# Optimization experiments

Hardware: AMD Instinct MI355X
Metric: run time of the kernel (lower is better)

## Reference

```python
import jax, jax.numpy as jnp
import numpy as np

L, B, I, H = 1024, 128, 256, 512

def setup_inputs() -> dict:
    key = jax.random.key(0)
    k1, k2, k3, k4, k5 = jax.random.split(key, 5)
    s_i = 1.0 / np.sqrt(I)
    s_h = 1.0 / np.sqrt(H)
    return {
        "x": jax.random.normal(k1, (L, B, I), dtype=jnp.float32),
        "h": jax.random.normal(k2, (B, H), dtype=jnp.float32),
        "Wx": jax.random.uniform(k3, (H, I), jnp.float32, -s_i, s_i),
        "Wh": jax.random.uniform(k4, (H, H), jnp.float32, -s_h, s_h),
        "bh": jax.random.uniform(k5, (H,), jnp.float32, -s_h, s_h),
    }

def reference(x, h, Wx, Wh, bh):
    # Precompute input projection for all timesteps as one big GEMM:
    # (L,B,I) @ (I,H) -> (L,B,H)
    xproj = jnp.einsum("lbi,hi->lbh", x, Wx)

    def step(h_prev, xp_t):
        h_new = jnp.tanh(xp_t + h_prev @ Wh.T + bh)  # (B,H)
        return h_new, h_new

    _, h_seq = jax.lax.scan(step, h, xproj)
    return h_seq  # (L, B, H)
```

## Files before the change

kernel.cpp:

```cpp
#include <hip/hip_runtime.h>

#define L_DIM 1024
#define B_DIM 128
#define I_DIM 256
#define H_DIM 512

typedef unsigned short u16x8 __attribute__((ext_vector_type(8)));
typedef __bf16 bf16x8 __attribute__((ext_vector_type(8)));
typedef float f32x4 __attribute__((ext_vector_type(4)));
typedef unsigned long long u64;
typedef unsigned int u32;
typedef u64 u64x2 __attribute__((ext_vector_type(2)));

static __device__ __forceinline__ unsigned short f2bf(float f) {
  unsigned u = __builtin_bit_cast(unsigned, f);
  u += 0x7FFFu + ((u >> 16) & 1u);
  return (unsigned short)(u >> 16);
}
static __device__ __forceinline__ float bf2f(unsigned short b) {
  return __builtin_bit_cast(float, ((unsigned)b) << 16);
}
static __device__ __forceinline__ bf16x8 ld_frag_g(const unsigned short* p, size_t idx8) {
  return __builtin_bit_cast(bf16x8, reinterpret_cast<const u16x8*>(p)[idx8]);
}

__global__ void pack_weights(const float* __restrict__ Wx, const float* __restrict__ Wh,
                             unsigned short* __restrict__ WxHi, unsigned short* __restrict__ WxLo,
                             unsigned short* __restrict__ WhHi, unsigned short* __restrict__ WhLo) {
  int tid = blockIdx.x * blockDim.x + threadIdx.x;
  if (tid < 32 * 8 * 64) {
    int lane = tid & 63, kt = (tid >> 6) & 7, nt = tid >> 9;
    int n = nt * 16 + (lane & 15), k0 = kt * 32 + (lane >> 4) * 8;
    const float* src = Wx + (size_t)n * I_DIM + k0;
    #pragma unroll
    for (int j = 0; j < 8; ++j) {
      float v = src[j];
      unsigned short hb = f2bf(v);
      WxHi[(size_t)tid * 8 + j] = hb;
      WxLo[(size_t)tid * 8 + j] = f2bf(v - bf2f(hb));
    }
  }
  if (tid < 32 * 16 * 64) {
    int lane = tid & 63, kt = (tid >> 6) & 15, nt = tid >> 10;
    int n = nt * 16 + (lane & 15), k0 = kt * 32 + (lane >> 4) * 8;
    const float* src = Wh + (size_t)n * H_DIM + k0;
    #pragma unroll
    for (int j = 0; j < 8; ++j) {
      float v = src[j];
      unsigned short hb = f2bf(v);
      WhHi[(size_t)tid * 8 + j] = hb;
      WhLo[(size_t)tid * 8 + j] = f2bf(v - bf2f(hb));
    }
  }
}

__global__ __launch_bounds__(256) void xproj_kernel(const float* __restrict__ x,
    const unsigned short* __restrict__ WxHi, const unsigned short* __restrict__ WxLo,
    const float* __restrict__ bh, float* __restrict__ out) {
  __shared__ unsigned short ahi[128][40];
  __shared__ unsigned short alo[128][40];
  const int tid = threadIdx.x, lane = tid & 63, wid = tid >> 6;
  const int mbase = blockIdx.x * 128, cbase = blockIdx.y * 128;
  const int wrow = (wid >> 1) * 64, wcol = (wid & 1) * 64;
  f32x4 acc[4][4] = {};
  const int srow = tid >> 1, shalf = (tid & 1) * 16;

  for (int kt = 0; kt < 8; ++kt) {
    const f32x4* src = reinterpret_cast<const f32x4*>(
        x + (size_t)(mbase + srow) * I_DIM + kt * 32 + shalf);
    f32x4 v[4];
    v[0] = src[0]; v[1] = src[1]; v[2] = src[2]; v[3] = src[3];
    u16x8 hh[2], ll[2];
    #pragma unroll
    for (int q = 0; q < 2; ++q) {
      #pragma unroll
      for (int e = 0; e < 8; ++e) {
        float f = v[q * 2 + (e >> 2)][e & 3];
        unsigned short hb = f2bf(f);
        hh[q][e] = hb;
        ll[q][e] = f2bf(f - bf2f(hb));
      }
    }
    __syncthreads();
    *reinterpret_cast<u16x8*>(&ahi[srow][shalf]) = hh[0];
    *reinterpret_cast<u16x8*>(&ahi[srow][shalf + 8]) = hh[1];
    *reinterpret_cast<u16x8*>(&alo[srow][shalf]) = ll[0];
    *reinterpret_cast<u16x8*>(&alo[srow][shalf + 8]) = ll[1];
    __syncthreads();

    bf16x8 amh[4], aml[4];
    #pragma unroll
    for (int m = 0; m < 4; ++m) {
      amh[m] = __builtin_bit_cast(bf16x8, *reinterpret_cast<const u16x8*>(
          &ahi[wrow + m * 16 + (lane & 15)][(lane >> 4) * 8]));
      aml[m] = __builtin_bit_cast(bf16x8, *reinterpret_cast<const u16x8*>(
          &alo[wrow + m * 16 + (lane & 15)][(lane >> 4) * 8]));
    }
    bf16x8 bhh[4], bll[4];
    #pragma unroll
    for (int n = 0; n < 4; ++n) {
      int ntg = (cbase + wcol) / 16 + n;
      size_t idx = (size_t)(ntg * 8 + kt) * 64 + lane;
      bhh[n] = ld_frag_g(WxHi, idx);
      bll[n] = ld_frag_g(WxLo, idx);
    }
    #pragma unroll
    for (int m = 0; m < 4; ++m) {
      #pragma unroll
      for (int n = 0; n < 4; ++n) {
        acc[m][n] = __builtin_amdgcn_mfma_f32_16x16x32_bf16(amh[m], bhh[n], acc[m][n], 0, 0, 0);
        acc[m][n] = __builtin_amdgcn_mfma_f32_16x16x32_bf16(aml[m], bhh[n], acc[m][n], 0, 0, 0);
        acc[m][n] = __builtin_amdgcn_mfma_f32_16x16x32_bf16(amh[m], bll[n], acc[m][n], 0, 0, 0);
      }
    }
  }

  #pragma unroll
  for (int n = 0; n < 4; ++n) {
    int col = cbase + wcol + n * 16 + (lane & 15);
    float bv = bh[col];
    #pragma unroll
    for (int m = 0; m < 4; ++m) {
      int rg = mbase + wrow + m * 16 + ((lane >> 4) << 2);
      #pragma unroll
      for (int r = 0; r < 4; ++r)
        out[(size_t)(rg + r) * H_DIM + col] = acc[m][n][r] + bv;
    }
  }
}

__global__ __launch_bounds__(64, 1) void rnn_kernel(const float* __restrict__ h0,
    const unsigned short* __restrict__ WhHi, const unsigned short* __restrict__ WhLo,
    u32* __restrict__ tags, unsigned short* __restrict__ slab,
    float* __restrict__ out) {
  const int lane = threadIdx.x & 63;
  const int b = blockIdx.x;
  const int g = b & 7, c = (b >> 3) & 7, w = (b >> 6) & 3;
  const int cw = c * 4 + w;

  bf16x8 wfh[16], wfl[16];
  #pragma unroll
  for (int kt = 0; kt < 16; ++kt) {
    size_t idx = (size_t)(cw * 16 + kt) * 64 + lane;
    wfh[kt] = ld_frag_g(WhHi, idx);
    wfl[kt] = ld_frag_g(WhLo, idx);
  }

  const int arow = lane & 15;
  const int aoff = (lane >> 4) * 8;
  const int drow = (lane >> 4) * 4;
  const int gcol = c * 64 + w * 16 + (lane & 15);
  const int koff2 = (lane >> 4) * 2;

  bf16x8 af[16];
  #pragma unroll
  for (int kt = 0; kt < 16; ++kt) {
    const f32x4* hp = reinterpret_cast<const f32x4*>(
        h0 + (size_t)(g * 16 + arow) * H_DIM + kt * 32 + aoff);
    f32x4 v0 = hp[0], v1 = hp[1];
    u16x8 hv;
    #pragma unroll
    for (int e = 0; e < 4; ++e) { hv[e] = f2bf(v0[e]); hv[4 + e] = f2bf(v1[e]); }
    af[kt] = __builtin_bit_cast(bf16x8, hv);
  }

  f32x4 xpv;
  #pragma unroll
  for (int r = 0; r < 4; ++r)
    xpv[r] = out[(size_t)(g * 16 + drow + r) * H_DIM + gcol];

  for (int t = 0; t < L_DIM; ++t) {
    const size_t obase = ((size_t)t * B_DIM + g * 16) * H_DIM;

    f32x4 a0 = {}, a1 = {}, a2 = {}, a3 = {};
    #pragma unroll
    for (int kt = 0; kt < 16; kt += 2) {
      a0 = __builtin_amdgcn_mfma_f32_16x16x32_bf16(af[kt], wfh[kt], a0, 0, 0, 0);
      a1 = __builtin_amdgcn_mfma_f32_16x16x32_bf16(af[kt], wfl[kt], a1, 0, 0, 0);
      a2 = __builtin_amdgcn_mfma_f32_16x16x32_bf16(af[kt + 1], wfh[kt + 1], a2, 0, 0, 0);
      a3 = __builtin_amdgcn_mfma_f32_16x16x32_bf16(af[kt + 1], wfl[kt + 1], a3, 0, 0, 0);
    }

    float hv[4]; unsigned short hu[4];
    #pragma unroll
    for (int r = 0; r < 4; ++r) {
      float z = a0[r] + a1[r] + a2[r] + a3[r] + xpv[r];
      float e = __expf(2.0f * z);
      hv[r] = 1.0f - 2.0f / (e + 1.0f);
      hu[r] = f2bf(hv[r]);
    }

    if (t < L_DIM - 1) {
      const unsigned step = (unsigned)(t + 1);
      const unsigned buf = step & 1;
      unsigned short* sg = slab + (size_t)(buf * 8 + g) * 8192;

      #pragma unroll
      for (int r = 0; r < 4; ++r)
        __hip_atomic_store(&sg[(drow + r) * H_DIM + gcol], hu[r],
                           __ATOMIC_RELAXED, __HIP_MEMORY_SCOPE_AGENT);
      __builtin_amdgcn_sched_barrier(0);
      asm volatile("s_waitcnt vmcnt(0)" ::: "memory");
      __builtin_amdgcn_sched_barrier(0);
      if (lane == 0)
        __hip_atomic_store(tags + ((size_t)(buf * 8 + g) * 32 + cw) * 16, step,
                           __ATOMIC_RELAXED, __HIP_MEMORY_SCOPE_AGENT);

      #pragma unroll
      for (int r = 0; r < 4; ++r)
        out[obase + (size_t)(drow + r) * H_DIM + gcol] = hv[r];
      const size_t obn = ((size_t)(t + 1) * B_DIM + g * 16) * H_DIM;
      #pragma unroll
      for (int r = 0; r < 4; ++r)
        xpv[r] = out[obn + (size_t)(drow + r) * H_DIM + gcol];

      if (lane < 32) {
        const u32* tp = tags + ((size_t)(buf * 8 + g) * 32 + lane) * 16;
        while (__hip_atomic_load(tp, __ATOMIC_RELAXED, __HIP_MEMORY_SCOPE_AGENT) < step) {}
      }
      __builtin_amdgcn_sched_barrier(0);
      asm volatile("" ::: "memory");

      const u64* sp = reinterpret_cast<const u64*>(sg);
      #pragma unroll
      for (int kt = 0; kt < 16; ++kt) {
        const u64* p = sp + arow * 128 + kt * 8 + koff2;
        u64x2 pv;
        pv[0] = __hip_atomic_load(p, __ATOMIC_RELAXED, __HIP_MEMORY_SCOPE_AGENT);
        pv[1] = __hip_atomic_load(p + 1, __ATOMIC_RELAXED, __HIP_MEMORY_SCOPE_AGENT);
        af[kt] = __builtin_bit_cast(bf16x8, pv);
      }
    } else {
      #pragma unroll
      for (int r = 0; r < 4; ++r)
        out[obase + (size_t)(drow + r) * H_DIM + gcol] = hv[r];
    }
  }
}

extern "C" void kernel_launch(void* const* d_in, const int* in_sizes, int n_in,
                              void* d_out, int out_size, void* d_ws, size_t ws_size,
                              hipStream_t stream) {
  (void)in_sizes; (void)n_in; (void)out_size; (void)ws_size;
  const float* x  = (const float*)d_in[0];
  const float* h0 = (const float*)d_in[1];
  const float* Wx = (const float*)d_in[2];
  const float* Wh = (const float*)d_in[3];
  const float* bh = (const float*)d_in[4];
  float* out = (float*)d_out;

  unsigned short* WxHi = (unsigned short*)d_ws;
  unsigned short* WxLo = WxHi + 131072;
  unsigned short* WhHi = WxLo + 131072;
  unsigned short* WhLo = WhHi + 262144;
  unsigned short* slab = (unsigned short*)((char*)d_ws + 1572864);
  u32*            tags = (u32*)((char*)d_ws + 1835008);

  hipMemsetAsync(tags, 0, 32768, stream);

  hipLaunchKernelGGL(pack_weights, dim3(128), dim3(256), 0, stream,
                     Wx, Wh, WxHi, WxLo, WhHi, WhLo);
  hipLaunchKernelGGL(xproj_kernel, dim3(1024, 4), dim3(256), 0, stream,
                     x, WxHi, WxLo, bh, out);
  hipLaunchKernelGGL(rnn_kernel, dim3(256), dim3(64), 0, stream,
                     h0, WhHi, WhLo, tags, slab, out);
}
```

Measured before the change: 3.220 ms.

## Embed step tags in slab data words to replace separate flag synchronization

```diff
diff --git a/kernel.cpp b/kernel.cpp
--- a/kernel.cpp
+++ b/kernel.cpp
@@ -10,7 +10,6 @@
 typedef float f32x4 __attribute__((ext_vector_type(4)));
 typedef unsigned long long u64;
 typedef unsigned int u32;
-typedef u64 u64x2 __attribute__((ext_vector_type(2)));
 
 static __device__ __forceinline__ unsigned short f2bf(float f) {
   unsigned u = __builtin_bit_cast(unsigned, f);
@@ -131,12 +130,10 @@
 
 __global__ __launch_bounds__(64, 1) void rnn_kernel(const float* __restrict__ h0,
     const unsigned short* __restrict__ WhHi, const unsigned short* __restrict__ WhLo,
-    u32* __restrict__ tags, unsigned short* __restrict__ slab,
-    float* __restrict__ out) {
+    u32* __restrict__ slab, float* __restrict__ out) {
   const int lane = threadIdx.x & 63;
   const int b = blockIdx.x;
-  const int g = b & 7, c = (b >> 3) & 7, w = (b >> 6) & 3;
-  const int cw = c * 4 + w;
+  const int g = b & 7, cw = (b >> 3) & 31;
 
   bf16x8 wfh[16], wfl[16];
   #pragma unroll
@@ -149,8 +146,7 @@
   const int arow = lane & 15;
   const int aoff = (lane >> 4) * 8;
   const int drow = (lane >> 4) * 4;
-  const int gcol = c * 64 + w * 16 + (lane & 15);
-  const int koff2 = (lane >> 4) * 2;
+  const int gcol = cw * 16 + (lane & 15);
 
   bf16x8 af[16];
   #pragma unroll
@@ -164,10 +160,13 @@
     af[kt] = __builtin_bit_cast(bf16x8, hv);
   }
 
-  f32x4 xpv;
+  f32x4 xpA, xpB;
   #pragma unroll
   for (int r = 0; r < 4; ++r)
-    xpv[r] = out[(size_t)(g * 16 + drow + r) * H_DIM + gcol];
+    xpA[r] = out[(size_t)(g * 16 + drow + r) * H_DIM + gcol];
+  #pragma unroll
+  for (int r = 0; r < 4; ++r)
+    xpB[r] = out[(size_t)B_DIM * H_DIM + (size_t)(g * 16 + drow + r) * H_DIM + gcol];
 
   for (int t = 0; t < L_DIM; ++t) {
     const size_t obase = ((size_t)t * B_DIM + g * 16) * H_DIM;
@@ -184,56 +183,68 @@
     float hv[4]; unsigned short hu[4];
     #pragma unroll
     for (int r = 0; r < 4; ++r) {
-      float z = a0[r] + a1[r] + a2[r] + a3[r] + xpv[r];
+      float z = a0[r] + a1[r] + a2[r] + a3[r] + xpA[r];
       float e = __expf(2.0f * z);
       hv[r] = 1.0f - 2.0f / (e + 1.0f);
       hu[r] = f2bf(hv[r]);
     }
 
-    if (t < L_DIM - 1) {
-      const unsigned step = (unsigned)(t + 1);
-      const unsigned buf = step & 1;
-      unsigned short* sg = slab + (size_t)(buf * 8 + g) * 8192;
-
-      #pragma unroll
-      for (int r = 0; r < 4; ++r)
-        __hip_atomic_store(&sg[(drow + r) * H_DIM + gcol], hu[r],
-                           __ATOMIC_RELAXED, __HIP_MEMORY_SCOPE_AGENT);
-      __builtin_amdgcn_sched_barrier(0);
-      asm volatile("s_waitcnt vmcnt(0)" ::: "memory");
-      __builtin_amdgcn_sched_barrier(0);
-      if (lane == 0)
-        __hip_atomic_store(tags + ((size_t)(buf * 8 + g) * 32 + cw) * 16, step,
-                           __ATOMIC_RELAXED, __HIP_MEMORY_SCOPE_AGENT);
-
+    if (t == L_DIM - 1) {
       #pragma unroll
       for (int r = 0; r < 4; ++r)
         out[obase + (size_t)(drow + r) * H_DIM + gcol] = hv[r];
-      const size_t obn = ((size_t)(t + 1) * B_DIM + g * 16) * H_DIM;
+      break;
+    }
+
+    const unsigned step = (unsigned)(t + 1);
+    u32* sg = slab + (size_t)((step & 1) * 8 + g) * 8192;
+    const u32 cbits = step << 16;
+
+    #pragma unroll
+    for (int r = 0; r < 4; ++r)
+      __hip_atomic_store(&sg[(drow + r) * 512 + gcol], cbits | (u32)hu[r],
+                         __ATOMIC_RELAXED, __HIP_MEMORY_SCOPE_AGENT);
+
+    #pragma unroll
+    for (int r = 0; r < 4; ++r)
+      out[obase + (size_t)(drow + r) * H_DIM + gcol] = hv[r];
+    xpA = xpB;
+    {
+      const int tn = (t + 2 < L_DIM) ? t + 2 : L_DIM - 1;
+      const size_t obn = ((size_t)tn * B_DIM + g * 16) * H_DIM;
       #pragma unroll
       for (int r = 0; r < 4; ++r)
-        xpv[r] = out[obn + (size_t)(drow + r) * H_DIM + gcol];
-
-      if (lane < 32) {
-        const u32* tp = tags + ((size_t)(buf * 8 + g) * 32 + lane) * 16;
-        while (__hip_atomic_load(tp, __ATOMIC_RELAXED, __HIP_MEMORY_SCOPE_AGENT) < step) {}
-      }
-      __builtin_amdgcn_sched_barrier(0);
-      asm volatile("" ::: "memory");
-
-      const u64* sp = reinterpret_cast<const u64*>(sg);
+        xpB[r] = out[obn + (size_t)(drow + r) * H_DIM + gcol];
+    }
+
+    const u64* base = reinterpret_cast<const u64*>(sg) + arow * 256 + (lane >> 4) * 4;
+    const u64 M = 0xFFFF0000FFFF0000ull;
+    const u64 E = (u64)step * 0x0001000000010000ull;
+    u64 pv[64];
+    bool ok;
+    do {
       #pragma unroll
       for (int kt = 0; kt < 16; ++kt) {
-        const u64* p = sp + arow * 128 + kt * 8 + koff2;
-        u64x2 pv;
-        pv[0] = __hip_atomic_load(p, __ATOMIC_RELAXED, __HIP_MEMORY_SCOPE_AGENT);
-        pv[1] = __hip_atomic_load(p + 1, __ATOMIC_RELAXED, __HIP_MEMORY_SCOPE_AGENT);
-        af[kt] = __builtin_bit_cast(bf16x8, pv);
-      }
-    } else {
-      #pragma unroll
-      for (int r = 0; r < 4; ++r)
-        out[obase + (size_t)(drow + r) * H_DIM + gcol] = hv[r];
+        #pragma unroll
+        for (int j = 0; j < 4; ++j)
+          pv[kt * 4 + j] = __hip_atomic_load(base + kt * 16 + j,
+                                             __ATOMIC_RELAXED, __HIP_MEMORY_SCOPE_AGENT);
+      }
+      ok = true;
+      #pragma unroll
+      for (int i = 0; i < 64; ++i) ok = ok && ((pv[i] & M) == E);
+    } while (!ok);
+
+    #pragma unroll
+    for (int kt = 0; kt < 16; ++kt) {
+      u16x8 w;
+      #pragma unroll
+      for (int j = 0; j < 4; ++j) {
+        u64 q = pv[kt * 4 + j];
+        w[2 * j] = (unsigned short)q;
+        w[2 * j + 1] = (unsigned short)(q >> 32);
+      }
+      af[kt] = __builtin_bit_cast(bf16x8, w);
     }
   }
 }
@@ -253,15 +264,12 @@
   unsigned short* WxLo = WxHi + 131072;
   unsigned short* WhHi = WxLo + 131072;
   unsigned short* WhLo = WhHi + 262144;
-  unsigned short* slab = (unsigned short*)((char*)d_ws + 1572864);
-  u32*            tags = (u32*)((char*)d_ws + 1835008);
-
-  hipMemsetAsync(tags, 0, 32768, stream);
+  u32* slab = (u32*)d_ws;
 
   hipLaunchKernelGGL(pack_weights, dim3(128), dim3(256), 0, stream,
                      Wx, Wh, WxHi, WxLo, WhHi, WhLo);
   hipLaunchKernelGGL(xproj_kernel, dim3(1024, 4), dim3(256), 0, stream,
                      x, WxHi, WxLo, bh, out);
   hipLaunchKernelGGL(rnn_kernel, dim3(256), dim3(64), 0, stream,
-                     h0, WhHi, WhLo, tags, slab, out);
-}
+                     h0, WhHi, WhLo, slab, out);
+}
```

Result: slower. 5.136 ms (+59.5%).

## Replace per-block tag flags with atomic counter barrier and double-buffer xproj prefetch

Applied to the files above, without the earlier changes.

```diff
diff --git a/kernel.cpp b/kernel.cpp
--- a/kernel.cpp
+++ b/kernel.cpp
@@ -131,12 +131,11 @@
 
 __global__ __launch_bounds__(64, 1) void rnn_kernel(const float* __restrict__ h0,
     const unsigned short* __restrict__ WhHi, const unsigned short* __restrict__ WhLo,
-    u32* __restrict__ tags, unsigned short* __restrict__ slab,
+    u32* __restrict__ ctr, unsigned short* __restrict__ slab,
     float* __restrict__ out) {
   const int lane = threadIdx.x & 63;
   const int b = blockIdx.x;
-  const int g = b & 7, c = (b >> 3) & 7, w = (b >> 6) & 3;
-  const int cw = c * 4 + w;
+  const int g = b & 7, cw = (b >> 3) & 31;
 
   bf16x8 wfh[16], wfl[16];
   #pragma unroll
@@ -149,8 +148,7 @@
   const int arow = lane & 15;
   const int aoff = (lane >> 4) * 8;
   const int drow = (lane >> 4) * 4;
-  const int gcol = c * 64 + w * 16 + (lane & 15);
-  const int koff2 = (lane >> 4) * 2;
+  const int gcol = cw * 16 + (lane & 15);
 
   bf16x8 af[16];
   #pragma unroll
@@ -164,10 +162,13 @@
     af[kt] = __builtin_bit_cast(bf16x8, hv);
   }
 
-  f32x4 xpv;
+  f32x4 xpA, xpB;
   #pragma unroll
   for (int r = 0; r < 4; ++r)
-    xpv[r] = out[(size_t)(g * 16 + drow + r) * H_DIM + gcol];
+    xpA[r] = out[(size_t)(g * 16 + drow + r) * H_DIM + gcol];
+  #pragma unroll
+  for (int r = 0; r < 4; ++r)
+    xpB[r] = out[(size_t)B_DIM * H_DIM + (size_t)(g * 16 + drow + r) * H_DIM + gcol];
 
   for (int t = 0; t < L_DIM; ++t) {
     const size_t obase = ((size_t)t * B_DIM + g * 16) * H_DIM;
@@ -184,56 +185,59 @@
     float hv[4]; unsigned short hu[4];
     #pragma unroll
     for (int r = 0; r < 4; ++r) {
-      float z = a0[r] + a1[r] + a2[r] + a3[r] + xpv[r];
+      float z = a0[r] + a1[r] + a2[r] + a3[r] + xpA[r];
       float e = __expf(2.0f * z);
       hv[r] = 1.0f - 2.0f / (e + 1.0f);
       hu[r] = f2bf(hv[r]);
     }
 
-    if (t < L_DIM - 1) {
-      const unsigned step = (unsigned)(t + 1);
-      const unsigned buf = step & 1;
-      unsigned short* sg = slab + (size_t)(buf * 8 + g) * 8192;
-
-      #pragma unroll
-      for (int r = 0; r < 4; ++r)
-        __hip_atomic_store(&sg[(drow + r) * H_DIM + gcol], hu[r],
-                           __ATOMIC_RELAXED, __HIP_MEMORY_SCOPE_AGENT);
-      __builtin_amdgcn_sched_barrier(0);
-      asm volatile("s_waitcnt vmcnt(0)" ::: "memory");
-      __builtin_amdgcn_sched_barrier(0);
-      if (lane == 0)
-        __hip_atomic_store(tags + ((size_t)(buf * 8 + g) * 32 + cw) * 16, step,
-                           __ATOMIC_RELAXED, __HIP_MEMORY_SCOPE_AGENT);
-
+    if (t == L_DIM - 1) {
       #pragma unroll
       for (int r = 0; r < 4; ++r)
         out[obase + (size_t)(drow + r) * H_DIM + gcol] = hv[r];
-      const size_t obn = ((size_t)(t + 1) * B_DIM + g * 16) * H_DIM;
+      break;
+    }
+
+    const unsigned step = (unsigned)(t + 1);
+    const unsigned buf = step & 1;
+    unsigned short* sg = slab + (size_t)(buf * 8 + g) * 8192;
+    u32* cp = ctr + (size_t)(buf * 8 + g) * 16;
+
+    #pragma unroll
+    for (int r = 0; r < 4; ++r)
+      __hip_atomic_store(&sg[(drow + r) * H_DIM + gcol], hu[r],
+                         __ATOMIC_RELAXED, __HIP_MEMORY_SCOPE_AGENT);
+    __builtin_amdgcn_sched_barrier(0);
+    asm volatile("s_waitcnt vmcnt(0)" ::: "memory");
+    __builtin_amdgcn_sched_barrier(0);
+    if (lane == 0)
+      __hip_atomic_fetch_add(cp, 1u, __ATOMIC_RELAXED, __HIP_MEMORY_SCOPE_AGENT);
+
+    #pragma unroll
+    for (int r = 0; r < 4; ++r)
+      out[obase + (size_t)(drow + r) * H_DIM + gcol] = hv[r];
+    xpA = xpB;
+    {
+      const int tn = (t + 2 < L_DIM) ? t + 2 : L_DIM - 1;
+      const size_t obn = ((size_t)tn * B_DIM + g * 16) * H_DIM;
       #pragma unroll
       for (int r = 0; r < 4; ++r)
-        xpv[r] = out[obn + (size_t)(drow + r) * H_DIM + gcol];
-
-      if (lane < 32) {
-        const u32* tp = tags + ((size_t)(buf * 8 + g) * 32 + lane) * 16;
-        while (__hip_atomic_load(tp, __ATOMIC_RELAXED, __HIP_MEMORY_SCOPE_AGENT) < step) {}
-      }
-      __builtin_amdgcn_sched_barrier(0);
-      asm volatile("" ::: "memory");
-
-      const u64* sp = reinterpret_cast<const u64*>(sg);
-      #pragma unroll
-      for (int kt = 0; kt < 16; ++kt) {
-        const u64* p = sp + arow * 128 + kt * 8 + koff2;
-        u64x2 pv;
-        pv[0] = __hip_atomic_load(p, __ATOMIC_RELAXED, __HIP_MEMORY_SCOPE_AGENT);
-        pv[1] = __hip_atomic_load(p + 1, __ATOMIC_RELAXED, __HIP_MEMORY_SCOPE_AGENT);
-        af[kt] = __builtin_bit_cast(bf16x8, pv);
-      }
-    } else {
-      #pragma unroll
-      for (int r = 0; r < 4; ++r)
-        out[obase + (size_t)(drow + r) * H_DIM + gcol] = hv[r];
+        xpB[r] = out[obn + (size_t)(drow + r) * H_DIM + gcol];
+    }
+
+    const u32 target = 32u * ((step + 1) >> 1);
+    while (__hip_atomic_load(cp, __ATOMIC_RELAXED, __HIP_MEMORY_SCOPE_AGENT) < target) {}
+    __builtin_amdgcn_sched_barrier(0);
+    asm volatile("" ::: "memory");
+
+    const u64* sp = reinterpret_cast<const u64*>(sg);
+    #pragma unroll
+    for (int kt = 0; kt < 16; ++kt) {
+      const u64* p = sp + arow * 128 + kt * 8 + (lane >> 4) * 2;
+      u64x2 pv2;
+      pv2[0] = __hip_atomic_load(p, __ATOMIC_RELAXED, __HIP_MEMORY_SCOPE_AGENT);
+      pv2[1] = __hip_atomic_load(p + 1, __ATOMIC_RELAXED, __HIP_MEMORY_SCOPE_AGENT);
+      af[kt] = __builtin_bit_cast(bf16x8, pv2);
     }
   }
 }
@@ -254,14 +258,14 @@
   unsigned short* WhHi = WxLo + 131072;
   unsigned short* WhLo = WhHi + 262144;
   unsigned short* slab = (unsigned short*)((char*)d_ws + 1572864);
-  u32*            tags = (u32*)((char*)d_ws + 1835008);
-
-  hipMemsetAsync(tags, 0, 32768, stream);
+  u32*            ctr  = (u32*)((char*)d_ws + 1835008);
+
+  hipMemsetAsync(ctr, 0, 1024, stream);
 
   hipLaunchKernelGGL(pack_weights, dim3(128), dim3(256), 0, stream,
                      Wx, Wh, WxHi, WxLo, WhHi, WhLo);
   hipLaunchKernelGGL(xproj_kernel, dim3(1024, 4), dim3(256), 0, stream,
                      x, WxHi, WxLo, bh, out);
   hipLaunchKernelGGL(rnn_kernel, dim3(256), dim3(64), 0, stream,
-                     h0, WhHi, WhLo, tags, slab, out);
-}
+                     h0, WhHi, WhLo, ctr, slab, out);
+}
```

Measured after the change: 3.261 ms. Within noise of the previous version (+1.3%).
